# Performance work log

Measured on AMD Instinct MI355X. Metric: run time of the kernel, lower is better.

## Reference

```python
import jax, jax.numpy as jnp
import numpy as np

B, IMG, P, D, NH, HS, L, V, TB, MLP, A = 32, 224, 16, 768, 12, 64, 12, 128, 32, 3072, 7
NPATCH = (IMG // P) ** 2          # 196 patches per image
SEQ = 1 + NPATCH + 1 + NPATCH + TB  # 426 = cls + obs + goal_tok + goal + lang


def _ln(x, g, b):
    m = x.mean(-1, keepdims=True)
    v = x.var(-1, keepdims=True)
    return (x - m) / jnp.sqrt(v + 1e-5) * g + b


def _patches(img):
    # einops 'b (h p1) (w p2) c -> b (h w) (p1 p2 c)'
    b = img.shape[0]
    h = IMG // P
    x = img.reshape(b, h, P, h, P, 3).transpose(0, 1, 3, 2, 4, 5)
    return x.reshape(b, h * h, P * P * 3)


def _forward(images, goal_imgs, goals_txt, patch_W, patch_b, tok_emb, pos_emb,
             cls_tok, goal_tok, Wq, Wk, Wv, Wo, bo, ln1_g, ln1_b, ln2_g, ln2_b,
             W1, b1, W2, b2, lnf_g, lnf_b, ah_W1, ah_b1, ah_W2, ah_b2):
    tok_obs = _patches(images) @ patch_W + patch_b        # [B, 196, D]
    tok_goal = _patches(goal_imgs) @ patch_W + patch_b    # [B, 196, D]
    tok_lang = tok_emb[goals_txt]                         # [B, 32, D]
    b = images.shape[0]
    x = jnp.concatenate([
        jnp.broadcast_to(cls_tok, (b, 1, D)),
        tok_obs,
        jnp.broadcast_to(goal_tok, (b, 1, D)),
        tok_goal,
        tok_lang,
    ], axis=1)                                            # [B, SEQ, D]
    x = x + pos_emb[None]
    scale = D ** -0.5  # NOTE: original Head scales by full n_embd, not head_size

    def block(x, p):
        wq, wk, wv, wo, bo_, l1g, l1b, l2g, l2b, w1, b1_, w2, b2_ = p
        xn = _ln(x, l1g, l1b)
        q = jnp.einsum('btd,hde->bhte', xn, wq)
        k = jnp.einsum('btd,hde->bhte', xn, wk)
        v = jnp.einsum('btd,hde->bhte', xn, wv)
        wei = jax.nn.softmax(jnp.einsum('bhte,bhse->bhts', q, k) * scale, axis=-1)
        att = jnp.einsum('bhts,bhse->bhte', wei, v)
        att = att.transpose(0, 2, 1, 3).reshape(x.shape[0], -1, D)  # concat heads
        x = x + att @ wo + bo_
        h = jax.nn.relu(_ln(x, l2g, l2b) @ w1 + b1_)
        x = x + h @ w2 + b2_
        return x, None

    x, _ = jax.lax.scan(block, x, (Wq, Wk, Wv, Wo, bo, ln1_g, ln1_b,
                                   ln2_g, ln2_b, W1, b1, W2, b2))
    x = _ln(x, lnf_g, lnf_b)
    cls = x[:, 0, :]
    out = jax.nn.relu(cls @ ah_W1 + ah_b1) @ ah_W2 + ah_b2  # [B, A]
    return out


def setup_inputs():
    key = jax.random.key(0)
    ks = jax.random.split(key, 20)
    nrm = lambda i, shape: 0.02 * jax.random.normal(ks[i], shape, dtype=jnp.float32)
    return {
        'images': jax.random.uniform(ks[0], (B, IMG, IMG, 3), dtype=jnp.float32),
        'goal_imgs': jax.random.uniform(ks[1], (B, IMG, IMG, 3), dtype=jnp.float32),
        'goals_txt': jax.random.randint(ks[2], (B, TB), 0, V, dtype=jnp.int32),
        'patch_W': nrm(3, (P * P * 3, D)), 'patch_b': jnp.zeros((D,), jnp.float32),
        'tok_emb': nrm(4, (V, D)),
        'pos_emb': nrm(5, (SEQ, D)),
        'cls_tok': jax.random.normal(ks[6], (1, 1, D), dtype=jnp.float32),
        'goal_tok': jax.random.normal(ks[7], (1, 1, D), dtype=jnp.float32),
        'Wq': nrm(8, (L, NH, D, HS)), 'Wk': nrm(9, (L, NH, D, HS)),
        'Wv': nrm(10, (L, NH, D, HS)),
        'Wo': nrm(11, (L, D, D)), 'bo': jnp.zeros((L, D), jnp.float32),
        'ln1_g': jnp.ones((L, D), jnp.float32), 'ln1_b': jnp.zeros((L, D), jnp.float32),
        'ln2_g': jnp.ones((L, D), jnp.float32), 'ln2_b': jnp.zeros((L, D), jnp.float32),
        'W1': nrm(12, (L, D, MLP)), 'b1': jnp.zeros((L, MLP), jnp.float32),
        'W2': nrm(13, (L, MLP, D)), 'b2': jnp.zeros((L, D), jnp.float32),
        'lnf_g': jnp.ones((D,), jnp.float32), 'lnf_b': jnp.zeros((D,), jnp.float32),
        'ah_W1': nrm(14, (D, 4 * D)), 'ah_b1': jnp.zeros((4 * D,), jnp.float32),
        'ah_W2': nrm(15, (4 * D, A)), 'ah_b2': jnp.zeros((A,), jnp.float32),
    }


def reference(images, goal_imgs, goals_txt, patch_W, patch_b, tok_emb, pos_emb,
              cls_tok, goal_tok, Wq, Wk, Wv, Wo, bo, ln1_g, ln1_b, ln2_g, ln2_b,
              W1, b1, W2, b2, lnf_g, lnf_b, ah_W1, ah_b1, ah_W2, ah_b2):
    return _forward(images, goal_imgs, goals_txt, patch_W, patch_b, tok_emb,
                    pos_emb, cls_tok, goal_tok, Wq, Wk, Wv, Wo, bo, ln1_g, ln1_b,
                    ln2_g, ln2_b, W1, b1, W2, b2, lnf_g, lnf_b, ah_W1, ah_b1,
                    ah_W2, ah_b2)
```

## Files before the change

### kernel.cpp

```cpp
#include <hip/hip_runtime.h>
#include <hip/hip_bf16.h>
#include <cstdint>

typedef __bf16 bf16x8 __attribute__((ext_vector_type(8)));
typedef __bf16 bf16x4v __attribute__((ext_vector_type(4)));
typedef float f32x4 __attribute__((ext_vector_type(4)));

static __device__ __forceinline__ f32x4 mfma16(bf16x8 a, bf16x8 b, f32x4 c) {
  return __builtin_amdgcn_mfma_f32_16x16x32_bf16(a, b, c, 0, 0, 0);
}
static __device__ __forceinline__ void gld_lds16(const void* g, void* l) {
  __builtin_amdgcn_global_load_lds(
      (__attribute__((address_space(1))) void*)(uintptr_t)g,
      (__attribute__((address_space(3))) void*)l, 16, 0, 0);
}

template <int EPI, int MODE>
__global__ __launch_bounds__(512, 2) void gemm256(
    const __bf16* __restrict__ A, const __bf16* __restrict__ Bt, int K, int ldc,
    int M, int nY,
    __bf16* __restrict__ outb, float* __restrict__ outf,
    const float* __restrict__ bias, const float* __restrict__ pos) {
  __shared__ __align__(16) __bf16 lds[4 * 16384];
  const int id = blockIdx.x;
  const int xcd = id & 7;
  const int j = id >> 3;
  const int rpx = (int)gridDim.x / (8 * nY);
  int bx, by;
  if (MODE == 0) { bx = xcd * rpx + j / nY; by = j % nY; }
  else           { by = j / rpx;            bx = xcd * rpx + j % rpx; }
  const long m0 = (long)bx * 256, n0 = (long)by * 256;
  if (m0 >= M) return;

  const int tid = threadIdx.x;
  const int wave = tid >> 6, lane = tid & 63;
  const int quad = lane >> 4, l16 = lane & 15;
  const int wm = wave >> 2, wn = wave & 3;

  const int gc = ((lane & 3) ^ ((lane >> 3) & 3)) * 8;
  const int srow = wave * 16 + (lane >> 2);
  const __bf16* gA0 = A + (m0 + srow) * (long)K + gc;
  const __bf16* gA1 = A + (m0 + 128 + srow) * (long)K + gc;
  const __bf16* gB0 = Bt + (n0 + srow) * (long)K + gc;
  const __bf16* gB1 = Bt + (n0 + 128 + srow) * (long)K + gc;
  const int ldw = wave * 1024;

  const int swz = (quad ^ ((l16 >> 1) & 3)) * 8;
  const int aoff = (wm * 128 + l16) * 32 + swz;
  const int boff = 8192 + (wn * 64 + l16) * 32 + swz;

  const f32x4 zz = {0.f, 0.f, 0.f, 0.f};
  f32x4 acc[8][4];
#pragma unroll
  for (int i = 0; i < 8; ++i)
#pragma unroll
    for (int jj = 0; jj < 4; ++jj) acc[i][jj] = zz;

  const int NT = K >> 5;

  auto stage = [&](int tt) {
    char* bb = (char*)lds + (tt & 3) * 32768 + ldw;
    const long ko = (long)tt * 32;
    gld_lds16(gA0 + ko, bb);
    gld_lds16(gA1 + ko, bb + 8192);
    gld_lds16(gB0 + ko, bb + 16384);
    gld_lds16(gB1 + ko, bb + 24576);
  };

  stage(0); stage(1); stage(2);
  asm volatile("s_waitcnt vmcnt(8)\n\ts_barrier" ::: "memory");

  for (int t = 0; t < NT; ++t) {
    if (t + 3 < NT) stage(t + 3);
    const __bf16* bb = lds + (t & 3) * 16384;
    bf16x8 af[8], bf[4];
#pragma unroll
    for (int mf = 0; mf < 8; ++mf) af[mf] = *(const bf16x8*)(bb + aoff + mf * 512);
#pragma unroll
    for (int nf = 0; nf < 4; ++nf) bf[nf] = *(const bf16x8*)(bb + boff + nf * 512);
    __builtin_amdgcn_s_setprio(1);
#pragma unroll
    for (int mf = 0; mf < 8; ++mf)
#pragma unroll
      for (int nf = 0; nf < 4; ++nf)
        acc[mf][nf] = mfma16(af[mf], bf[nf], acc[mf][nf]);
    __builtin_amdgcn_s_setprio(0);
    if (t + 1 < NT) {
      if (t + 4 <= NT)      asm volatile("s_waitcnt vmcnt(8)\n\ts_barrier" ::: "memory");
      else if (t + 3 == NT) asm volatile("s_waitcnt vmcnt(4)\n\ts_barrier" ::: "memory");
      else                  asm volatile("s_waitcnt vmcnt(0)\n\ts_barrier" ::: "memory");
    }
  }

#pragma unroll
  for (int mf = 0; mf < 8; ++mf) {
#pragma unroll
    for (int r = 0; r < 4; ++r) {
      const long row = m0 + wm * 128 + mf * 16 + quad * 4 + r;
      if (row >= M) continue;
      if (EPI == 3) {
        const int rr = (int)row;
        const int gsel = rr >= 6272 ? 1 : 0;
        const int rm = rr - gsel * 6272;
        const int bb2 = rm / 196, pp = rm % 196;
        const int tpos = gsel ? (198 + pp) : (1 + pp);
        float* xr = outf + ((long)bb2 * 426 + tpos) * 768;
        const float* pr = pos + (long)tpos * 768;
#pragma unroll
        for (int nf = 0; nf < 4; ++nf) {
          const long col = n0 + wn * 64 + nf * 16 + l16;
          xr[col] = acc[mf][nf][r] + bias[col] + pr[col];
        }
      } else {
#pragma unroll
        for (int nf = 0; nf < 4; ++nf) {
          const long col = n0 + wn * 64 + nf * 16 + l16;
          const float v = acc[mf][nf][r];
          if (EPI == 0) outb[row * ldc + col] = (__bf16)v;
          else if (EPI == 1) outb[row * ldc + col] = (__bf16)fmaxf(v + bias[col], 0.f);
          else outf[row * ldc + col] += v + bias[col];
        }
      }
    }
  }
}

__global__ __launch_bounds__(256) void transpose_pack(
    const float* __restrict__ in, __bf16* __restrict__ out, int K, int N,
    int nh, long out_ls, long out_hs) {
  __shared__ float tile[32][33];
  const int z = blockIdx.z;
  const long in_o = (long)z * K * N;
  const long out_o = (long)(z / nh) * out_ls + (long)(z % nh) * out_hs;
  const int n0 = blockIdx.x * 32, k0 = blockIdx.y * 32;
  const int tx = threadIdx.x, ty = threadIdx.y;
#pragma unroll
  for (int i = 0; i < 4; ++i)
    tile[ty + i * 8][tx] = in[in_o + (long)(k0 + ty + i * 8) * N + n0 + tx];
  __syncthreads();
#pragma unroll
  for (int i = 0; i < 4; ++i)
    out[out_o + (long)(n0 + ty + i * 8) * K + k0 + tx] = (__bf16)tile[tx][ty + i * 8];
}

__global__ __launch_bounds__(256) void patches_k(const float* __restrict__ img0,
                                                 const float* __restrict__ img1,
                                                 __bf16* __restrict__ out) {
  const int row = blockIdx.x;
  const int gsel = row >= 6272 ? 1 : 0;
  const int rm = row - gsel * 6272;
  const int b = rm / 196, p = rm % 196;
  const int py = p / 14, px = p % 14;
  const float* img = gsel ? img1 : img0;
#pragma unroll
  for (int i = 0; i < 3; ++i) {
    const int k = threadIdx.x + i * 256;
    const int pidx = k / 3, c = k - pidx * 3;
    const int pr = pidx >> 4, pc = pidx & 15;
    const float v = img[(((long)b * 224 + py * 16 + pr) * 224 + px * 16 + pc) * 3 + c];
    out[(long)row * 768 + k] = (__bf16)v;
  }
}

__global__ __launch_bounds__(256) void assemble_k(
    const float* __restrict__ cls_tok, const float* __restrict__ goal_tok,
    const float* __restrict__ tok_emb, const int* __restrict__ txt,
    const float* __restrict__ pos, float* __restrict__ x) {
  const int z = blockIdx.x;
  const int b = z / 34, j = z % 34;
  const int t = (j == 0) ? 0 : (j == 1) ? 197 : (392 + j);
  const float* src = (j == 0) ? cls_tok
                   : (j == 1) ? goal_tok
                              : tok_emb + (long)txt[b * 32 + (j - 2)] * 768;
  float* dst = x + ((long)b * 426 + t) * 768;
  const float* pr = pos + (long)t * 768;
#pragma unroll
  for (int i = 0; i < 3; ++i) {
    const int k = threadIdx.x + i * 256;
    dst[k] = src[k] + pr[k];
  }
}

template <int CLS>
__global__ __launch_bounds__(64) void ln_k(const float* __restrict__ x,
                                           const float* __restrict__ g,
                                           const float* __restrict__ b,
                                           __bf16* __restrict__ out) {
  const int row = blockIdx.x, lane = threadIdx.x;
  const long irow = CLS ? (long)row * 426 : (long)row;
  const float4* xr = (const float4*)(x + irow * 768);
  float4 v[3];
  float s = 0.f, q = 0.f;
#pragma unroll
  for (int i = 0; i < 3; ++i) {
    v[i] = xr[lane + i * 64];
    s += v[i].x + v[i].y + v[i].z + v[i].w;
    q += v[i].x * v[i].x + v[i].y * v[i].y + v[i].z * v[i].z + v[i].w * v[i].w;
  }
#pragma unroll
  for (int o = 32; o > 0; o >>= 1) {
    s += __shfl_xor(s, o);
    q += __shfl_xor(q, o);
  }
  const float mean = s * (1.f / 768.f);
  const float var = q * (1.f / 768.f) - mean * mean;
  const float rs = rsqrtf(var + 1e-5f);
  const float4* g4 = (const float4*)g;
  const float4* b4 = (const float4*)b;
#pragma unroll
  for (int i = 0; i < 3; ++i) {
    const float4 gg = g4[lane + i * 64], bb = b4[lane + i * 64];
    bf16x4v o4;
    o4[0] = (__bf16)((v[i].x - mean) * rs * gg.x + bb.x);
    o4[1] = (__bf16)((v[i].y - mean) * rs * gg.y + bb.y);
    o4[2] = (__bf16)((v[i].z - mean) * rs * gg.z + bb.z);
    o4[3] = (__bf16)((v[i].w - mean) * rs * gg.w + bb.w);
    *(bf16x4v*)(out + (long)row * 768 + (lane + i * 64) * 4) = o4;
  }
}

__global__ __launch_bounds__(256) void vtrans_k(const __bf16* __restrict__ qkv,
                                                __bf16* __restrict__ vt) {
  __shared__ __bf16 tile[64][66];
  const int bh = blockIdx.x;
  const int b = bh / 12, h = bh % 12;
  const int s0 = blockIdx.y * 64;
  const int t = threadIdx.x;
  const int sr = t >> 2, part = t & 3;
  const __bf16* src = qkv + ((long)(b * 426 + s0 + sr)) * 2304 + 1536 + h * 64 + part * 16;
#pragma unroll
  for (int j = 0; j < 16; ++j) tile[sr][part * 16 + j] = src[j];
  __syncthreads();
  __bf16* dst = vt + ((long)bh * 64 + sr) * 448 + s0 + part * 16;
#pragma unroll
  for (int j = 0; j < 16; ++j) {
    const int s = s0 + part * 16 + j;
    dst[j] = (s < 426) ? tile[part * 16 + j][sr] : (__bf16)0.f;
  }
}

__global__ __launch_bounds__(256) void attn_k(const __bf16* __restrict__ qkv,
                                              const __bf16* __restrict__ vt,
                                              __bf16* __restrict__ attout) {
  __shared__ __align__(16) __bf16 lds[8192 + 4096];
  const int tid = threadIdx.x;
  const int wave = tid >> 6, lane = tid & 63;
  const int quad = lane >> 4, l16 = lane & 15;
  const int bh = blockIdx.x;
  const int b = bh / 12, h = bh % 12;
  const int q0 = blockIdx.y * 64 + wave * 16;
  const long b426 = (long)b * 426;

  const int swz0 = ((quad) ^ (l16 & 7)) * 8;
  const int swz1 = ((4 + quad) ^ (l16 & 7)) * 8;
  __bf16* lsK = lds;
  __bf16* lsV = lds + 4096;
  __bf16* lsP = lds + 8192 + wave * 1024;

  const __bf16* gsrc[4];
  long gstep[4];
#pragma unroll
  for (int s = 0; s < 4; ++s) {
    const int c = s * 256 + tid;
    if (c < 512) {
      const int key = c >> 3, part = (c & 7) ^ (key & 7);
      gsrc[s] = qkv + (b426 + key) * 2304 + 768 + h * 64 + part * 8;
      gstep[s] = 64 * 2304;
    } else {
      const int cv = c - 512;
      const int e = cv >> 3, part = (cv & 7) ^ (e & 7);
      gsrc[s] = vt + ((long)bh * 64 + e) * 448 + part * 8;
      gstep[s] = 64;
    }
  }
  __bf16* ldst[4];
#pragma unroll
  for (int s = 0; s < 4; ++s) ldst[s] = lds + (s * 256 + (tid & ~63)) * 8;

  const long qrow = (b426 + q0 + l16) * 2304 + h * 64;
  const bf16x8 aq0 = *(const bf16x8*)(qkv + qrow + quad * 8);
  const bf16x8 aq1 = *(const bf16x8*)(qkv + qrow + 32 + quad * 8);

  const f32x4 zz = {0.f, 0.f, 0.f, 0.f};
  f32x4 o[4] = {zz, zz, zz, zz};
  float m_i[4] = {-3e38f, -3e38f, -3e38f, -3e38f};
  float l_i[4] = {0.f, 0.f, 0.f, 0.f};
  const float scale = 0.03608439182435161f;

  for (int kc = 0; kc < 7; ++kc) {
    const int kbase = kc * 64;
    __syncthreads();
#pragma unroll
    for (int s = 0; s < 4; ++s) {
      gld_lds16(gsrc[s], ldst[s]);
      gsrc[s] += gstep[s];
    }
    __syncthreads();

    f32x4 s4[4] = {zz, zz, zz, zz};
#pragma unroll
    for (int nt = 0; nt < 4; ++nt) {
      const __bf16* kb = lsK + (nt * 16 + l16) * 64;
      s4[nt] = mfma16(aq0, *(const bf16x8*)(kb + swz0), s4[nt]);
      s4[nt] = mfma16(aq1, *(const bf16x8*)(kb + swz1), s4[nt]);
    }

    const int lim = 426 - kbase - l16;
#pragma unroll
    for (int r = 0; r < 4; ++r) {
      float a0 = (0 < lim)  ? s4[0][r] * scale : -1e30f;
      float a1 = (16 < lim) ? s4[1][r] * scale : -1e30f;
      float a2 = (32 < lim) ? s4[2][r] * scale : -1e30f;
      float a3 = (48 < lim) ? s4[3][r] * scale : -1e30f;
      float mx = fmaxf(fmaxf(a0, a1), fmaxf(a2, a3));
#pragma unroll
      for (int w = 1; w < 16; w <<= 1) mx = fmaxf(mx, __shfl_xor(mx, w, 16));
      mx = fmaxf(mx, m_i[r]);
      const float alpha = __expf(m_i[r] - mx);
      m_i[r] = mx;
      const float p0 = __expf(a0 - mx), p1 = __expf(a1 - mx);
      const float p2 = __expf(a2 - mx), p3 = __expf(a3 - mx);
      float rs = (p0 + p1) + (p2 + p3);
#pragma unroll
      for (int w = 1; w < 16; w <<= 1) rs += __shfl_xor(rs, w, 16);
      l_i[r] = l_i[r] * alpha + rs;
      o[0][r] *= alpha; o[1][r] *= alpha; o[2][r] *= alpha; o[3][r] *= alpha;
      const int rowb = quad * 4 + r;
      __bf16* pb = lsP + rowb * 64 + (l16 & 7);
      const int l8 = l16 >> 3, rx = rowb & 7;
      pb[((0 + l8) ^ rx) * 8] = (__bf16)p0;
      pb[((2 + l8) ^ rx) * 8] = (__bf16)p1;
      pb[((4 + l8) ^ rx) * 8] = (__bf16)p2;
      pb[((6 + l8) ^ rx) * 8] = (__bf16)p3;
    }

    const bf16x8 pa0 = *(const bf16x8*)(lsP + l16 * 64 + swz0);
    const bf16x8 pa1 = *(const bf16x8*)(lsP + l16 * 64 + swz1);
#pragma unroll
    for (int et = 0; et < 4; ++et) {
      const __bf16* vb = lsV + (et * 16 + l16) * 64;
      o[et] = mfma16(pa0, *(const bf16x8*)(vb + swz0), o[et]);
      o[et] = mfma16(pa1, *(const bf16x8*)(vb + swz1), o[et]);
    }
  }

#pragma unroll
  for (int r = 0; r < 4; ++r) {
    const int q = q0 + quad * 4 + r;
    if (q < 426) {
      const float inv = 1.f / l_i[r];
      __bf16* dst = attout + (b426 + q) * 768 + h * 64 + l16;
#pragma unroll
      for (int et = 0; et < 4; ++et) dst[et * 16] = (__bf16)(o[et][r] * inv);
    }
  }
}

__global__ __launch_bounds__(256) void head1_k(const __bf16* __restrict__ cls,
                                               const float* __restrict__ W1,
                                               const float* __restrict__ b1,
                                               float* __restrict__ hh) {
  __shared__ float red[4][64];
  const int blk = blockIdx.x;
  const int r = blk / 48, nt = blk % 48;
  const int tid = threadIdx.x;
  const int kq = tid >> 6, nl = tid & 63;
  const int n = nt * 64 + nl;
  const __bf16* c = cls + (long)r * 768 + kq * 192;
  const float* w = W1 + (long)(kq * 192) * 3072 + n;
  float s = 0.f;
#pragma unroll 4
  for (int k = 0; k < 192; ++k) s += (float)c[k] * w[(long)k * 3072];
  if (kq) red[kq][nl] = s;
  __syncthreads();
  if (kq == 0) {
    s += red[1][nl] + red[2][nl] + red[3][nl];
    hh[(long)r * 3072 + n] = fmaxf(s + b1[n], 0.f);
  }
}

__global__ __launch_bounds__(64) void head2_k(const float* __restrict__ hh,
                                              const float* __restrict__ W2,
                                              const float* __restrict__ b2,
                                              float* __restrict__ out) {
  const int o = blockIdx.x;
  const int r = o / 7, n = o % 7;
  const int lane = threadIdx.x;
  const float* hr = hh + (long)r * 3072;
  float s = 0.f;
  for (int k = lane; k < 3072; k += 64) s += hr[k] * W2[(long)k * 7 + n];
#pragma unroll
  for (int off = 32; off > 0; off >>= 1) s += __shfl_xor(s, off);
  if (lane == 0) out[o] = s + b2[n];
}

extern "C" void kernel_launch(void* const* d_in, const int* in_sizes, int n_in,
                              void* d_out, int out_size, void* d_ws, size_t ws_size,
                              hipStream_t stream) {
  (void)in_sizes; (void)n_in; (void)out_size; (void)ws_size;
  const float* images   = (const float*)d_in[0];
  const float* goal_img = (const float*)d_in[1];
  const int*   txt      = (const int*)d_in[2];
  const float* patch_W  = (const float*)d_in[3];
  const float* patch_b  = (const float*)d_in[4];
  const float* tok_emb  = (const float*)d_in[5];
  const float* pos_emb  = (const float*)d_in[6];
  const float* cls_tok  = (const float*)d_in[7];
  const float* goal_tok = (const float*)d_in[8];
  const float* Wq   = (const float*)d_in[9];
  const float* Wk   = (const float*)d_in[10];
  const float* Wv   = (const float*)d_in[11];
  const float* Wo   = (const float*)d_in[12];
  const float* bo   = (const float*)d_in[13];
  const float* ln1g = (const float*)d_in[14];
  const float* ln1b = (const float*)d_in[15];
  const float* ln2g = (const float*)d_in[16];
  const float* ln2b = (const float*)d_in[17];
  const float* W1   = (const float*)d_in[18];
  const float* b1   = (const float*)d_in[19];
  const float* W2   = (const float*)d_in[20];
  const float* b2   = (const float*)d_in[21];
  const float* lnfg = (const float*)d_in[22];
  const float* lnfb = (const float*)d_in[23];
  const float* aW1  = (const float*)d_in[24];
  const float* ab1  = (const float*)d_in[25];
  const float* aW2  = (const float*)d_in[26];
  const float* ab2  = (const float*)d_in[27];

  char* base = (char*)d_ws;
  size_t off = 0;
  auto take = [&](size_t bytes) -> char* {
    char* p = base + off;
    off += (bytes + 255) & ~(size_t)255;
    return p;
  };
  float*  x     = (float*) take((size_t)13696 * 768 * 4);
  __bf16* xn    = (__bf16*)take((size_t)13696 * 768 * 2);
  __bf16* shard = (__bf16*)take((size_t)13696 * 3072 * 2);
  __bf16* attb  = (__bf16*)take((size_t)13696 * 768 * 2);
  __bf16* vt    = (__bf16*)take((size_t)384 * 64 * 448 * 2);
  float*  hh    = (float*) take((size_t)32 * 3072 * 4);
  __bf16* wqkv  = (__bf16*)take((size_t)12 * 2304 * 768 * 2);
  __bf16* wot   = (__bf16*)take((size_t)12 * 768 * 768 * 2);
  __bf16* w1t   = (__bf16*)take((size_t)12 * 768 * 3072 * 2);
  __bf16* w2t   = (__bf16*)take((size_t)12 * 768 * 3072 * 2);
  __bf16* pwt   = (__bf16*)take((size_t)768 * 768 * 2);
  __bf16* qkv   = shard;
  __bf16* hbuf  = shard;
  __bf16* patches = shard;

  const dim3 tpb(32, 8);
  transpose_pack<<<dim3(24, 24, 1), tpb, 0, stream>>>(patch_W, pwt, 768, 768, 1, 0L, 0L);
  transpose_pack<<<dim3(2, 24, 144), tpb, 0, stream>>>(Wq, wqkv, 768, 64, 12, 1769472L, 49152L);
  transpose_pack<<<dim3(2, 24, 144), tpb, 0, stream>>>(Wk, wqkv + 589824, 768, 64, 12, 1769472L, 49152L);
  transpose_pack<<<dim3(2, 24, 144), tpb, 0, stream>>>(Wv, wqkv + 1179648, 768, 64, 12, 1769472L, 49152L);
  transpose_pack<<<dim3(24, 24, 12), tpb, 0, stream>>>(Wo, wot, 768, 768, 1, 589824L, 0L);
  transpose_pack<<<dim3(96, 24, 12), tpb, 0, stream>>>(W1, w1t, 768, 3072, 1, 2359296L, 0L);
  transpose_pack<<<dim3(24, 96, 12), tpb, 0, stream>>>(W2, w2t, 3072, 768, 1, 2359296L, 0L);

  patches_k<<<12544, 256, 0, stream>>>(images, goal_img, patches);
  assemble_k<<<1088, 256, 0, stream>>>(cls_tok, goal_tok, tok_emb, txt, pos_emb, x);
  gemm256<3, 1><<<8 * 7 * 3, 512, 0, stream>>>(patches, pwt, 768, 768, 12544, 3,
                                               nullptr, x, patch_b, pos_emb);

  for (int l = 0; l < 12; ++l) {
    ln_k<0><<<13696, 64, 0, stream>>>(x, ln1g + l * 768, ln1b + l * 768, xn);
    gemm256<0, 1><<<8 * 7 * 9, 512, 0, stream>>>(xn, wqkv + (long)l * 1769472, 768, 2304,
                                                 13696, 9, qkv, nullptr, nullptr, nullptr);
    vtrans_k<<<dim3(384, 7), 256, 0, stream>>>(qkv, vt);
    attn_k<<<dim3(384, 7), 256, 0, stream>>>(qkv, vt, attb);
    gemm256<2, 1><<<8 * 7 * 3, 512, 0, stream>>>(attb, wot + (long)l * 589824, 768, 768,
                                                 13696, 3, nullptr, x, bo + l * 768, nullptr);
    ln_k<0><<<13696, 64, 0, stream>>>(x, ln2g + l * 768, ln2b + l * 768, xn);
    gemm256<1, 1><<<8 * 7 * 12, 512, 0, stream>>>(xn, w1t + (long)l * 2359296, 768, 3072,
                                                  13696, 12, hbuf, nullptr, b1 + l * 3072, nullptr);
    gemm256<2, 0><<<8 * 7 * 3, 512, 0, stream>>>(hbuf, w2t + (long)l * 2359296, 3072, 768,
                                                 13696, 3, nullptr, x, b2 + l * 768, nullptr);
  }
  ln_k<1><<<32, 64, 0, stream>>>(x, lnfg, lnfb, xn);
  head1_k<<<1536, 256, 0, stream>>>(xn, aW1, ab1, hh);
  head2_k<<<224, 64, 0, stream>>>(hh, aW2, ab2, (float*)d_out);
}
```

Measured before the change: 5.588 ms.

## Store GEMM A-operands in K-blocked 32-column panels for contiguous tile loads

```diff
diff --git a/kernel.cpp b/kernel.cpp
--- a/kernel.cpp
+++ b/kernel.cpp
@@ -5,6 +5,8 @@
 typedef __bf16 bf16x8 __attribute__((ext_vector_type(8)));
 typedef __bf16 bf16x4v __attribute__((ext_vector_type(4)));
 typedef float f32x4 __attribute__((ext_vector_type(4)));
+
+#define XROWS 13696L
 
 static __device__ __forceinline__ f32x4 mfma16(bf16x8 a, bf16x8 b, f32x4 c) {
   return __builtin_amdgcn_mfma_f32_16x16x32_bf16(a, b, c, 0, 0, 0);
@@ -15,7 +17,7 @@
       (__attribute__((address_space(3))) void*)l, 16, 0, 0);
 }
 
-template <int EPI, int MODE>
+template <int EPI, int MODE, int PACKA>
 __global__ __launch_bounds__(512, 2) void gemm256(
     const __bf16* __restrict__ A, const __bf16* __restrict__ Bt, int K, int ldc,
     int M, int nY,
@@ -39,8 +41,17 @@
 
   const int gc = ((lane & 3) ^ ((lane >> 3) & 3)) * 8;
   const int srow = wave * 16 + (lane >> 2);
-  const __bf16* gA0 = A + (m0 + srow) * (long)K + gc;
-  const __bf16* gA1 = A + (m0 + 128 + srow) * (long)K + gc;
+  const __bf16 *gA0, *gA1;
+  long aStep;
+  if (PACKA) {
+    gA0 = A + (m0 + srow) * 32 + gc;
+    gA1 = A + (m0 + 128 + srow) * 32 + gc;
+    aStep = XROWS * 32;
+  } else {
+    gA0 = A + (m0 + srow) * (long)K + gc;
+    gA1 = A + (m0 + 128 + srow) * (long)K + gc;
+    aStep = 32;
+  }
   const __bf16* gB0 = Bt + (n0 + srow) * (long)K + gc;
   const __bf16* gB1 = Bt + (n0 + 128 + srow) * (long)K + gc;
   const int ldw = wave * 1024;
@@ -60,11 +71,12 @@
 
   auto stage = [&](int tt) {
     char* bb = (char*)lds + (tt & 3) * 32768 + ldw;
-    const long ko = (long)tt * 32;
-    gld_lds16(gA0 + ko, bb);
-    gld_lds16(gA1 + ko, bb + 8192);
-    gld_lds16(gB0 + ko, bb + 16384);
-    gld_lds16(gB1 + ko, bb + 24576);
+    const long ka = (long)tt * aStep;
+    const long kb = (long)tt * 32;
+    gld_lds16(gA0 + ka, bb);
+    gld_lds16(gA1 + ka, bb + 8192);
+    gld_lds16(gB0 + kb, bb + 16384);
+    gld_lds16(gB1 + kb, bb + 24576);
   };
 
   stage(0); stage(1); stage(2);
@@ -117,7 +129,9 @@
           const long col = n0 + wn * 64 + nf * 16 + l16;
           const float v = acc[mf][nf][r];
           if (EPI == 0) outb[row * ldc + col] = (__bf16)v;
-          else if (EPI == 1) outb[row * ldc + col] = (__bf16)fmaxf(v + bias[col], 0.f);
+          else if (EPI == 1)
+            outb[((col >> 5) * XROWS + row) * 32 + (col & 31)] =
+                (__bf16)fmaxf(v + bias[col], 0.f);
           else outf[row * ldc + col] += v + bias[col];
         }
       }
@@ -215,7 +229,11 @@
     o4[1] = (__bf16)((v[i].y - mean) * rs * gg.y + bb.y);
     o4[2] = (__bf16)((v[i].z - mean) * rs * gg.z + bb.z);
     o4[3] = (__bf16)((v[i].w - mean) * rs * gg.w + bb.w);
-    *(bf16x4v*)(out + (long)row * 768 + (lane + i * 64) * 4) = o4;
+    const int e0 = (lane + i * 64) * 4;
+    if (CLS)
+      *(bf16x4v*)(out + (long)row * 768 + e0) = o4;
+    else
+      *(bf16x4v*)(out + ((long)(e0 >> 5) * XROWS + row) * 32 + (e0 & 31)) = o4;
   }
 }
 
@@ -349,9 +367,13 @@
     const int q = q0 + quad * 4 + r;
     if (q < 426) {
       const float inv = 1.f / l_i[r];
-      __bf16* dst = attout + (b426 + q) * 768 + h * 64 + l16;
-#pragma unroll
-      for (int et = 0; et < 4; ++et) dst[et * 16] = (__bf16)(o[et][r] * inv);
+      const long row = b426 + q;
+#pragma unroll
+      for (int et = 0; et < 4; ++et) {
+        const int col = h * 64 + et * 16 + l16;
+        attout[((long)(col >> 5) * XROWS + row) * 32 + (col & 31)] =
+            (__bf16)(o[et][r] * inv);
+      }
     }
   }
 }
@@ -439,6 +461,7 @@
   __bf16* shard = (__bf16*)take((size_t)13696 * 3072 * 2);
   __bf16* attb  = (__bf16*)take((size_t)13696 * 768 * 2);
   __bf16* vt    = (__bf16*)take((size_t)384 * 64 * 448 * 2);
+  __bf16* xcls  = (__bf16*)take((size_t)32 * 768 * 2);
   float*  hh    = (float*) take((size_t)32 * 3072 * 4);
   __bf16* wqkv  = (__bf16*)take((size_t)12 * 2304 * 768 * 2);
   __bf16* wot   = (__bf16*)take((size_t)12 * 768 * 768 * 2);
@@ -460,24 +483,24 @@
 
   patches_k<<<12544, 256, 0, stream>>>(images, goal_img, patches);
   assemble_k<<<1088, 256, 0, stream>>>(cls_tok, goal_tok, tok_emb, txt, pos_emb, x);
-  gemm256<3, 1><<<8 * 7 * 3, 512, 0, stream>>>(patches, pwt, 768, 768, 12544, 3,
-                                               nullptr, x, patch_b, pos_emb);
+  gemm256<3, 1, 0><<<8 * 7 * 3, 512, 0, stream>>>(patches, pwt, 768, 768, 12544, 3,
+                                                  nullptr, x, patch_b, pos_emb);
 
   for (int l = 0; l < 12; ++l) {
     ln_k<0><<<13696, 64, 0, stream>>>(x, ln1g + l * 768, ln1b + l * 768, xn);
-    gemm256<0, 1><<<8 * 7 * 9, 512, 0, stream>>>(xn, wqkv + (long)l * 1769472, 768, 2304,
-                                                 13696, 9, qkv, nullptr, nullptr, nullptr);
+    gemm256<0, 1, 1><<<8 * 7 * 9, 512, 0, stream>>>(xn, wqkv + (long)l * 1769472, 768, 2304,
+                                                    13696, 9, qkv, nullptr, nullptr, nullptr);
     vtrans_k<<<dim3(384, 7), 256, 0, stream>>>(qkv, vt);
     attn_k<<<dim3(384, 7), 256, 0, stream>>>(qkv, vt, attb);
-    gemm256<2, 1><<<8 * 7 * 3, 512, 0, stream>>>(attb, wot + (long)l * 589824, 768, 768,
-                                                 13696, 3, nullptr, x, bo + l * 768, nullptr);
+    gemm256<2, 1, 1><<<8 * 7 * 3, 512, 0, stream>>>(attb, wot + (long)l * 589824, 768, 768,
+                                                    13696, 3, nullptr, x, bo + l * 768, nullptr);
     ln_k<0><<<13696, 64, 0, stream>>>(x, ln2g + l * 768, ln2b + l * 768, xn);
-    gemm256<1, 1><<<8 * 7 * 12, 512, 0, stream>>>(xn, w1t + (long)l * 2359296, 768, 3072,
-                                                  13696, 12, hbuf, nullptr, b1 + l * 3072, nullptr);
-    gemm256<2, 0><<<8 * 7 * 3, 512, 0, stream>>>(hbuf, w2t + (long)l * 2359296, 3072, 768,
-                                                 13696, 3, nullptr, x, b2 + l * 768, nullptr);
-  }
-  ln_k<1><<<32, 64, 0, stream>>>(x, lnfg, lnfb, xn);
-  head1_k<<<1536, 256, 0, stream>>>(xn, aW1, ab1, hh);
+    gemm256<1, 1, 1><<<8 * 7 * 12, 512, 0, stream>>>(xn, w1t + (long)l * 2359296, 768, 3072,
+                                                     13696, 12, hbuf, nullptr, b1 + l * 3072, nullptr);
+    gemm256<2, 0, 1><<<8 * 7 * 3, 512, 0, stream>>>(hbuf, w2t + (long)l * 2359296, 3072, 768,
+                                                    13696, 3, nullptr, x, b2 + l * 768, nullptr);
+  }
+  ln_k<1><<<32, 64, 0, stream>>>(x, lnfg, lnfb, xcls);
+  head1_k<<<1536, 256, 0, stream>>>(xcls, aW1, ab1, hh);
   head2_k<<<224, 64, 0, stream>>>(hh, aW2, ab2, (float*)d_out);
 }
```

New measurement: 5.503 ms. About the same (-1.5%).
